# Performance work log

Measured on AMD Instinct MI355X. Metric: run time of the kernel, lower is better.

Reference implementation:

```python
import jax, jax.numpy as jnp
import numpy as np

N = 10000   # num_nodes
F = 64      # latent_dim
U = 128     # num_units
B = 8       # batch
K = 2       # gcn_step
E = 160000  # edges (avg degree 16)
M = 2 * K + 1  # num_matrices = len(supports)*gcn_step + 1


def setup_inputs() -> dict:
    rng = np.random.default_rng(0)
    rows = rng.integers(0, N, E).astype(np.int32)
    cols = rng.integers(0, N, E).astype(np.int32)
    vals = (rng.random(E).astype(np.float32) + 0.1)
    # random-walk normalization D^{-1} A, per the original utils.calculate_random_walk_matrix
    deg_out = np.zeros(N, np.float32); np.add.at(deg_out, rows, vals)
    deg_in = np.zeros(N, np.float32); np.add.at(deg_in, cols, vals)
    # support1 = (D_out^{-1} A)^T : out[c] += vals/d_out[r] * x[r]  -> dst=cols, src=rows
    w1 = vals / np.maximum(deg_out[rows], 1e-8)
    # support2 = (D_in^{-1} A^T)^T : out[r] += vals/d_in[c] * x[c]  -> dst=rows, src=cols
    w2 = vals / np.maximum(deg_in[cols], 1e-8)

    key = jax.random.key(0)
    ks = jax.random.split(key, 4)

    def xavier(k, shape):
        std = (2.0 / (shape[0] + shape[1])) ** 0.5
        return jax.random.normal(k, shape, jnp.float32) * std

    return {
        'y': jax.random.normal(ks[0], (B, N * F), jnp.float32),
        'W_lat': xavier(ks[1], (M * F, F)),
        'b_lat': jnp.ones((F,), jnp.float32),   # bias_start=1.0, shared (keyed by length)
        'W_units': xavier(ks[2], (M * F, U)),
        'b_units': jnp.zeros((U,), jnp.float32),
        'W_final': xavier(ks[3], (M * U, F)),
        'sup1_w': jnp.asarray(w1),
        'sup2_w': jnp.asarray(w2),
        'edge_rows': jnp.asarray(rows),
        'edge_cols': jnp.asarray(cols),
    }


def _spmm(dst, src, w, x):
    # sparse matmul S @ x with S given as COO edge list; x: (N, Fin, B)
    return jax.ops.segment_sum(w[:, None, None] * x[src], dst, num_segments=N)


def _gconv(x, supports, W, b):
    # x: (B, N, Fin) -> (B, N*Fout); Chebyshev diffusion convolution
    Bsz, n, fin = x.shape
    x0 = jnp.transpose(x, (1, 2, 0))  # (N, Fin, B)
    xs = [x0]
    for dst, src, w in supports:
        xk_2 = x0
        x1 = _spmm(dst, src, w, x0)
        xs.append(x1)
        for _ in range(2, K + 1):
            x2 = 2.0 * _spmm(dst, src, w, x1) - xk_2
            xs.append(x2)
            xk_2, x1 = x1, x2
    X = jnp.stack(xs, axis=-1)                       # (N, Fin, B, M)
    X = jnp.transpose(X, (2, 0, 1, 3)).reshape(Bsz * n, fin * len(xs))  # feature-major, matrix-minor
    out = X @ W + b
    return out.reshape(Bsz, n * W.shape[1])


def reference(y, W_lat, b_lat, W_units, b_units, W_final, sup1_w, sup2_w, edge_rows, edge_cols):
    supports = [(edge_cols, edge_rows, sup1_w), (edge_rows, edge_cols, sup2_w)]
    x = y.reshape(B, N, F)
    # theta gate (bias_start=1.0 via shared b_lat)
    theta = jax.nn.sigmoid(_gconv(x, supports, W_lat, b_lat))
    # ode_func_net: gen_layers=1 hidden gconv + final gconv (final bias is shared b_lat!)
    c = jnp.tanh(_gconv(x, supports, W_units, b_units)).reshape(B, N, U)
    c = jnp.tanh(_gconv(c, supports, W_final, b_lat))
    return -theta * c
```

## Files before the change

kernel.cpp:

```cpp
#include <hip/hip_runtime.h>

#define N_NODES 10000
#define NEDGE 160000
#define NB 80000
#define EPAD (NEDGE + 8 * N_NODES)

typedef unsigned int u32;
typedef unsigned short u16;
typedef __attribute__((ext_vector_type(8))) short short8;
typedef __attribute__((ext_vector_type(4))) float float4v;

__device__ __forceinline__ u16 f2bf(float f) {
    u32 u = __float_as_uint(f);
    return (u16)((u + 0x7fffu + ((u >> 16) & 1u)) >> 16);
}
__device__ __forceinline__ float lo16(u32 u) { return __uint_as_float(u << 16); }
__device__ __forceinline__ float hi16(u32 u) { return __uint_as_float(u & 0xffff0000u); }
__device__ __forceinline__ u32 pack2(float a, float b) {
    return (u32)f2bf(a) | (((u32)f2bf(b)) << 16);
}
__device__ __forceinline__ float fast_tanh(float v) {
    return 1.f - 2.f / (__expf(2.f * v) + 1.f);
}

static const size_t SLAB = (size_t)NB * 64;

__global__ __launch_bounds__(256) void prepcount_kernel(
    const float2* __restrict__ y, u32* __restrict__ X0,
    const float* __restrict__ W_lat, const float* __restrict__ W_units,
    u16* __restrict__ bpk12, const float* __restrict__ W_final, u16* __restrict__ bpkP,
    const int* __restrict__ rows, const int* __restrict__ cols, int* __restrict__ cnt) {
    int b = blockIdx.x, t = threadIdx.x;
    if (b < 10000) {
        int idx = b * 256 + t;
        int fh = idx & 31;
        int rb = idx >> 5;
        int bb = rb & 7;
        int n = rb >> 3;
        float2 v = y[((size_t)bb * N_NODES + n) * 32 + fh];
        X0[idx] = pack2(v.x, v.y);
    } else if (b < 10240) {
        int idx = (b - 10000) * 256 + t;
        int j = idx & 7;
        int lane = (idx >> 3) & 63;
        int rest = idx >> 9;
        int ct = rest % 12;
        int ks = rest / 12;
        int k = ks * 32 + (lane >> 4) * 8 + j;
        int col = ct * 16 + (lane & 15);
        int wrow = (k % 64) * 5 + (k / 64);
        float v = (col < 64) ? W_lat[wrow * 64 + col] : W_units[wrow * 128 + (col - 64)];
        bpk12[idx] = f2bf(v);
    } else if (b < 10400) {
        int idx = (b - 10240) * 256 + t;
        int j8 = idx & 7;
        int lane = (idx >> 3) & 63;
        int rest = idx >> 9;
        int ct = rest % 20;
        int ks = rest / 20;
        int k = ks * 32 + (lane >> 4) * 8 + j8;
        int col = ct * 16 + (lane & 15);
        int slot = col >> 6, j = col & 63;
        float v;
        if (slot == 0)
            v = W_final[(k * 5 + 0) * 64 + j] - W_final[(k * 5 + 2) * 64 + j] -
                W_final[(k * 5 + 4) * 64 + j];
        else
            v = W_final[(k * 5 + slot) * 64 + j];
        bpkP[idx] = f2bf(v);
    } else {
        int e = (b - 10400) * 256 + t;
        atomicAdd(&cnt[cols[e]], 1);
        atomicAdd(&cnt[N_NODES + rows[e]], 1);
    }
}

__global__ void blocksum_kernel(const int* __restrict__ cnt, int* __restrict__ bsums) {
    __shared__ int red[4];
    int arr = blockIdx.x / 40;
    int c = blockIdx.x % 40;
    int idx = c * 256 + threadIdx.x;
    int v = (idx < N_NODES) ? ((cnt[arr * N_NODES + idx] + 7) & ~7) : 0;
#pragma unroll
    for (int off = 32; off; off >>= 1) v += __shfl_down(v, off, 64);
    int wv = threadIdx.x >> 6, ln = threadIdx.x & 63;
    if (ln == 0) red[wv] = v;
    __syncthreads();
    if (threadIdx.x == 0) bsums[blockIdx.x] = red[0] + red[1] + red[2] + red[3];
}

__global__ void scanapply_kernel(int* __restrict__ cnt, const int* __restrict__ bsums,
                                 int* __restrict__ rowptr1, int* __restrict__ rowptr2) {
    __shared__ int lds[256];
    int arr = blockIdx.x / 40;
    int c = blockIdx.x % 40;
    int base = 0;
    for (int i = 0; i < c; i++) base += bsums[arr * 40 + i];
    int idx = c * 256 + threadIdx.x;
    bool ok = idx < N_NODES;
    int v = ok ? ((cnt[arr * N_NODES + idx] + 7) & ~7) : 0;
    int t = threadIdx.x;
    lds[t] = v;
    __syncthreads();
    for (int off = 1; off < 256; off <<= 1) {
        int add = (t >= off) ? lds[t - off] : 0;
        __syncthreads();
        lds[t] += add;
        __syncthreads();
    }
    int excl = lds[t] - v + base;
    if (ok) {
        int* rp = arr ? rowptr2 : rowptr1;
        rp[idx] = excl;
        cnt[arr * N_NODES + idx] = excl;
    }
    if (c == 39 && t == 255) {
        (arr ? rowptr2 : rowptr1)[N_NODES] = base + lds[255];
    }
}

__global__ void scatter_kernel(const int* __restrict__ rows, const int* __restrict__ cols,
                               const float* __restrict__ w1, const float* __restrict__ w2,
                               int* __restrict__ cur1, int* __restrict__ cur2,
                               int2* __restrict__ edges1, int2* __restrict__ edges2) {
    int e = blockIdx.x * 256 + threadIdx.x;
    if (e < NEDGE) {
        int r = rows[e], c = cols[e];
        int p1 = atomicAdd(&cur1[c], 1);
        edges1[p1] = make_int2(r, __float_as_int(w1[e]));
        int p2 = atomicAdd(&cur2[r], 1);
        edges2[p2] = make_int2(c, __float_as_int(w2[e]));
    }
}

__device__ __forceinline__ void gacc(float* acc, float w, uint4 u) {
    acc[0] += w * lo16(u.x); acc[1] += w * hi16(u.x);
    acc[2] += w * lo16(u.y); acc[3] += w * hi16(u.y);
    acc[4] += w * lo16(u.z); acc[5] += w * hi16(u.z);
    acc[6] += w * lo16(u.w); acc[7] += w * hi16(u.w);
}

__device__ __forceinline__ void gather_sliced(const u32* __restrict__ Xin,
                                              const int* __restrict__ rp,
                                              const int2* __restrict__ eg,
                                              int row, bool valid, int su, int l,
                                              float* acc) {
    int e = 0, e1 = 0;
    if (valid) {
        e = rp[row] + l;
        e1 = rp[row + 1];
    }
    while (__ballot(e < e1)) {
        int2 me = make_int2(0, 0);
        if (e < e1) me = eg[e];
#pragma unroll
        for (int j = 0; j < 8; j++) {
            int s = __shfl(me.x, j, 8);
            float w = __int_as_float(__shfl(me.y, j, 8));
            uint4 u = *(const uint4*)(Xin + (size_t)s * 256 + su + l * 4);
            gacc(acc, w, u);
        }
        e += 8;
    }
}

__global__ __launch_bounds__(256) void spmm2_kernel(
    const u32* __restrict__ XinA, const u32* __restrict__ XprevA, u32* __restrict__ XoutA,
    const u32* __restrict__ XinB, const u32* __restrict__ XprevB, u32* __restrict__ XoutB,
    const int* __restrict__ rowptr1, const int2* __restrict__ edges1,
    const int* __restrict__ rowptr2, const int2* __restrict__ edges2,
    float alpha, float beta) {
    int t = threadIdx.x;
    int lane = t & 63;
    int g = lane >> 3, l = lane & 7;
    int slice = blockIdx.x & 7;
    int chunk = blockIdx.x >> 3;
    int su = slice * 32;
    int v = chunk * 32 + (t >> 6) * 8 + g;
    bool hB = v >= N_NODES;
    int n = hB ? v - N_NODES : v;
    const u32* Xin = hB ? XinB : XinA;
    const u32* Xprev = hB ? XprevB : XprevA;
    u32* Xout = hB ? XoutB : XoutA;
    const int* rp = hB ? rowptr2 : rowptr1;
    const int2* eg = hB ? edges2 : edges1;

    float acc[8] = {0.f, 0.f, 0.f, 0.f, 0.f, 0.f, 0.f, 0.f};
    gather_sliced(Xin, rp, eg, n, true, su, l, acc);

    size_t o = (size_t)n * 256 + su + l * 4;
    if (beta != 0.f) {
        uint4 p = *(const uint4*)(Xprev + o);
        acc[0] = alpha * acc[0] + beta * lo16(p.x); acc[1] = alpha * acc[1] + beta * hi16(p.x);
        acc[2] = alpha * acc[2] + beta * lo16(p.y); acc[3] = alpha * acc[3] + beta * hi16(p.y);
        acc[4] = alpha * acc[4] + beta * lo16(p.z); acc[5] = alpha * acc[5] + beta * hi16(p.z);
        acc[6] = alpha * acc[6] + beta * lo16(p.w); acc[7] = alpha * acc[7] + beta * hi16(p.w);
    } else {
#pragma unroll
        for (int i = 0; i < 8; i++) acc[i] *= alpha;
    }
    uint4 r;
    r.x = pack2(acc[0], acc[1]);
    r.y = pack2(acc[2], acc[3]);
    r.z = pack2(acc[4], acc[5]);
    r.w = pack2(acc[6], acc[7]);
    *(uint4*)(Xout + o) = r;
}

__global__ __launch_bounds__(256) void spmm_final_kernel(
    const u32* __restrict__ T1, const u32* __restrict__ T2,
    const u32* __restrict__ Q, const u32* __restrict__ theta,
    const int* __restrict__ rowptr1, const int2* __restrict__ edges1,
    const int* __restrict__ rowptr2, const int2* __restrict__ edges2,
    float* __restrict__ outF) {
    int t = threadIdx.x;
    int lane = t & 63;
    int g = lane >> 3, l = lane & 7;
    int slice = blockIdx.x & 7;
    int chunk = blockIdx.x >> 3;
    int su = slice * 32;
    int n = chunk * 32 + (t >> 6) * 8 + g;
    bool valid = n < N_NODES;

    float acc[8] = {0.f, 0.f, 0.f, 0.f, 0.f, 0.f, 0.f, 0.f};
    gather_sliced(T1, rowptr1, edges1, n, valid, su, l, acc);
    gather_sliced(T2, rowptr2, edges2, n, valid, su, l, acc);
    if (!valid) return;

    size_t o = (size_t)n * 256 + su + l * 4;
    uint4 q = *(const uint4*)(Q + o);
    uint4 th = *(const uint4*)(theta + o);
    float res[8];
    res[0] = -lo16(th.x) * fast_tanh(lo16(q.x) + acc[0]);
    res[1] = -hi16(th.x) * fast_tanh(hi16(q.x) + acc[1]);
    res[2] = -lo16(th.y) * fast_tanh(lo16(q.y) + acc[2]);
    res[3] = -hi16(th.y) * fast_tanh(hi16(q.y) + acc[3]);
    res[4] = -lo16(th.z) * fast_tanh(lo16(q.z) + acc[4]);
    res[5] = -hi16(th.z) * fast_tanh(hi16(q.z) + acc[5]);
    res[6] = -lo16(th.w) * fast_tanh(lo16(q.w) + acc[6]);
    res[7] = -hi16(th.w) * fast_tanh(hi16(q.w) + acc[7]);
    float* dst = outF + (size_t)slice * (N_NODES * 64) + (size_t)n * 64 + l * 8;
    *(float4*)(dst) = make_float4(res[0], res[1], res[2], res[3]);
    *(float4*)(dst + 4) = make_float4(res[4], res[5], res[6], res[7]);
}

struct Slabs { const u16* p[5]; };

template <int FIN, int NM, int NOUT, int NSPLIT, int MODE>
__global__ __launch_bounds__(256) void gemm_kernel(
    Slabs A, const u16* __restrict__ Bp, const float* __restrict__ bias1,
    const float* __restrict__ bias2, u16* __restrict__ O1, u16* __restrict__ O2) {
    constexpr int K = NM * FIN;
    constexpr int KS = K / 32;
    constexpr int CTT = NOUT / 16;
    constexpr int CT = CTT / NSPLIT;
    int lane = threadIdx.x & 63;
    int wave = threadIdx.x >> 6;
    int rowBase = (blockIdx.x / NSPLIT) * 64 + wave * 16;
    int ctBase = (blockIdx.x % NSPLIT) * CT;
    int mrow = lane & 15;
    int kq = lane >> 4;

    float4v acc[CT];
#pragma unroll
    for (int c = 0; c < CT; c++) acc[c] = (float4v){0.f, 0.f, 0.f, 0.f};

#pragma unroll
    for (int ks = 0; ks < KS; ks++) {
        int k = ks * 32 + kq * 8;
        int m = k / FIN;
        int koff = k % FIN;
        short8 a = *(const short8*)(A.p[m] + (size_t)(rowBase + mrow) * FIN + koff);
        short8 b[CT];
#pragma unroll
        for (int ct = 0; ct < CT; ct++)
            b[ct] = *(const short8*)(Bp + ((size_t)(ks * CTT + ctBase + ct) * 64 + lane) * 8);
#pragma unroll
        for (int ct = 0; ct < CT; ct++)
            acc[ct] = __builtin_amdgcn_mfma_f32_16x16x32_bf16(a, b[ct], acc[ct], 0, 0, 0);
    }

    int rowq = rowBase + kq * 4;
#pragma unroll
    for (int ct = 0; ct < CT; ct++) {
        int col = (ctBase + ct) * 16 + mrow;
        float bsv;
        if (MODE == 0) bsv = (col < 64) ? bias1[col] : 0.f;
        else bsv = (col < 64) ? bias1[col] : bias2[col - 64];
#pragma unroll
        for (int i = 0; i < 4; i++) {
            float v = acc[ct][i] + bsv;
            int r = rowq + i;
            if (MODE == 0) {
                O1[(size_t)(col >> 6) * SLAB + (size_t)r * 64 + (col & 63)] = f2bf(v);
            } else {
                if (col < 64) {
                    v = 1.f / (1.f + __expf(-v));
                    O1[(size_t)r * 64 + col] = f2bf(v);
                } else {
                    O2[(size_t)r * 128 + (col - 64)] = f2bf(fast_tanh(v));
                }
            }
        }
    }
}

extern "C" void kernel_launch(void* const* d_in, const int* in_sizes, int n_in,
                              void* d_out, int out_size, void* d_ws, size_t ws_size,
                              hipStream_t stream) {
    const float2* y    = (const float2*)d_in[0];
    const float* W_lat = (const float*)d_in[1];
    const float* b_lat = (const float*)d_in[2];
    const float* W_units = (const float*)d_in[3];
    const float* b_units = (const float*)d_in[4];
    const float* W_final = (const float*)d_in[5];
    const float* sup1w = (const float*)d_in[6];
    const float* sup2w = (const float*)d_in[7];
    const int* rows    = (const int*)d_in[8];
    const int* cols    = (const int*)d_in[9];
    float* out = (float*)d_out;

    char* ws = (char*)d_ws;
    size_t off = 0;
    auto alloc = [&](size_t bytes) -> void* {
        void* p = ws + off;
        off += (bytes + 511) & ~(size_t)511;
        return p;
    };
    int* rowptr1 = (int*)alloc((N_NODES + 1) * 4);
    int* rowptr2 = (int*)alloc((N_NODES + 1) * 4);
    int* cnt = (int*)alloc((size_t)2 * N_NODES * 4);
    int* bsums = (int*)alloc(80 * 4);
    int2* edges1 = (int2*)alloc((size_t)EPAD * 8);
    int2* edges2 = (int2*)alloc((size_t)EPAD * 8);
    u16* bpk12 = (u16*)alloc((size_t)61440 * 2);
    u16* bpkP = (u16*)alloc((size_t)40960 * 2);
    u16* theta = (u16*)alloc((size_t)NB * 64 * 2);
    u16* S = (u16*)alloc((size_t)5 * NB * 64 * 2);
    u16* H0 = (u16*)alloc((size_t)NB * 128 * 2);
    u16* T1 = (u16*)alloc((size_t)NB * 64 * 2);
    u16* T2 = (u16*)alloc((size_t)NB * 64 * 2);

    hipMemsetAsync(cnt, 0, (size_t)2 * N_NODES * 4, stream);
    hipMemsetAsync(edges1, 0, (size_t)EPAD * 8, stream);
    hipMemsetAsync(edges2, 0, (size_t)EPAD * 8, stream);
    prepcount_kernel<<<11025, 256, 0, stream>>>(y, (u32*)S, W_lat, W_units, bpk12,
                                                W_final, bpkP, rows, cols, cnt);
    blocksum_kernel<<<80, 256, 0, stream>>>(cnt, bsums);
    scanapply_kernel<<<80, 256, 0, stream>>>(cnt, bsums, rowptr1, rowptr2);
    scatter_kernel<<<625, 256, 0, stream>>>(rows, cols, sup1w, sup2w,
                                            cnt, cnt + N_NODES, edges1, edges2);

    const u32* S0 = (const u32*)S;
    u32* X1 = (u32*)(S + 1 * SLAB);
    u32* X2 = (u32*)(S + 2 * SLAB);
    u32* X3 = (u32*)(S + 3 * SLAB);
    u32* X4 = (u32*)(S + 4 * SLAB);
    spmm2_kernel<<<5000, 256, 0, stream>>>(S0, nullptr, X1, S0, nullptr, X3,
                                           rowptr1, edges1, rowptr2, edges2, 1.f, 0.f);
    spmm2_kernel<<<5000, 256, 0, stream>>>(X1, S0, X2, X3, S0, X4,
                                           rowptr1, edges1, rowptr2, edges2, 2.f, -1.f);

    Slabs SX;
    for (int m = 0; m < 5; m++) SX.p[m] = S + (size_t)m * SLAB;
    gemm_kernel<64, 5, 192, 1, 1><<<1250, 256, 0, stream>>>(SX, bpk12, b_lat, b_units, theta, H0);

    Slabs SH;
    SH.p[0] = H0;
    gemm_kernel<128, 1, 320, 2, 0><<<2500, 256, 0, stream>>>(SH, bpkP, b_lat, nullptr, S, nullptr);

    const u32* Q  = (const u32*)(S + 0 * SLAB);
    const u32* P1 = (const u32*)(S + 1 * SLAB);
    const u32* P2 = (const u32*)(S + 2 * SLAB);
    const u32* P3 = (const u32*)(S + 3 * SLAB);
    const u32* P4 = (const u32*)(S + 4 * SLAB);
    spmm2_kernel<<<5000, 256, 0, stream>>>(P2, P1, (u32*)T1, P4, P3, (u32*)T2,
                                           rowptr1, edges1, rowptr2, edges2, 2.f, 1.f);
    spmm_final_kernel<<<2504, 256, 0, stream>>>((const u32*)T1, (const u32*)T2, Q,
                                                (const u32*)theta,
                                                rowptr1, edges1, rowptr2, edges2, out);
}
```

Before: 314.1 us.

## Bucket nodes by degree so SpMM wavefronts process similar-length rows

Builds per-support node orderings sorted by edge-count bucket (descending) via a histogram, a serial scan and an atomic fill, then has the SpMM kernels map threads to nodes through these permutations. The aim is to cut intra-wavefront divergence, since 8 nodes share a wavefront and run the gather loop for as many steps as the longest row. The cost is two extra small launches, extra histogram work in the scatter kernel, and one indirection load per thread. Output rows are also no longer written in node order, which may reduce locality.

```diff
diff --git a/kernel.cpp b/kernel.cpp
--- a/kernel.cpp
+++ b/kernel.cpp
@@ -122,14 +122,52 @@
 __global__ void scatter_kernel(const int* __restrict__ rows, const int* __restrict__ cols,
                                const float* __restrict__ w1, const float* __restrict__ w2,
                                int* __restrict__ cur1, int* __restrict__ cur2,
-                               int2* __restrict__ edges1, int2* __restrict__ edges2) {
-    int e = blockIdx.x * 256 + threadIdx.x;
-    if (e < NEDGE) {
+                               int2* __restrict__ edges1, int2* __restrict__ edges2,
+                               const int* __restrict__ rp1, const int* __restrict__ rp2,
+                               int* __restrict__ hist) {
+    if (blockIdx.x < 625) {
+        int e = blockIdx.x * 256 + threadIdx.x;
         int r = rows[e], c = cols[e];
         int p1 = atomicAdd(&cur1[c], 1);
         edges1[p1] = make_int2(r, __float_as_int(w1[e]));
         int p2 = atomicAdd(&cur2[r], 1);
         edges2[p2] = make_int2(c, __float_as_int(w2[e]));
+    } else {
+        int n = (blockIdx.x - 625) * 256 + threadIdx.x;
+        if (n < N_NODES) {
+            int c1 = min(31, (rp1[n + 1] - rp1[n]) >> 3);
+            int c2 = min(31, (rp2[n + 1] - rp2[n]) >> 3);
+            int c12 = min(31, c1 + c2);
+            atomicAdd(&hist[c1], 1);
+            atomicAdd(&hist[32 + c2], 1);
+            atomicAdd(&hist[64 + c12], 1);
+        }
+    }
+}
+
+__global__ void orderscan_kernel(int* __restrict__ histcur) {
+    if (threadIdx.x == 0) {
+        for (int a = 0; a < 3; a++) {
+            int base = 0;
+            for (int b = 31; b >= 0; b--) {
+                histcur[96 + a * 32 + b] = base;
+                base += histcur[a * 32 + b];
+            }
+        }
+    }
+}
+
+__global__ void orderfill_kernel(const int* __restrict__ rp1, const int* __restrict__ rp2,
+                                 int* __restrict__ histcur, int* __restrict__ order1,
+                                 int* __restrict__ order2, int* __restrict__ order12) {
+    int n = blockIdx.x * 256 + threadIdx.x;
+    if (n < N_NODES) {
+        int c1 = min(31, (rp1[n + 1] - rp1[n]) >> 3);
+        int c2 = min(31, (rp2[n + 1] - rp2[n]) >> 3);
+        int c12 = min(31, c1 + c2);
+        order1[atomicAdd(&histcur[96 + c1], 1)] = n;
+        order2[atomicAdd(&histcur[96 + 32 + c2], 1)] = n;
+        order12[atomicAdd(&histcur[96 + 64 + c12], 1)] = n;
     }
 }
 
@@ -169,6 +207,7 @@
     const u32* __restrict__ XinB, const u32* __restrict__ XprevB, u32* __restrict__ XoutB,
     const int* __restrict__ rowptr1, const int2* __restrict__ edges1,
     const int* __restrict__ rowptr2, const int2* __restrict__ edges2,
+    const int* __restrict__ order1, const int* __restrict__ order2,
     float alpha, float beta) {
     int t = threadIdx.x;
     int lane = t & 63;
@@ -178,7 +217,7 @@
     int su = slice * 32;
     int v = chunk * 32 + (t >> 6) * 8 + g;
     bool hB = v >= N_NODES;
-    int n = hB ? v - N_NODES : v;
+    int n = hB ? order2[v - N_NODES] : order1[v];
     const u32* Xin = hB ? XinB : XinA;
     const u32* Xprev = hB ? XprevB : XprevA;
     u32* Xout = hB ? XoutB : XoutA;
@@ -212,15 +251,16 @@
     const u32* __restrict__ Q, const u32* __restrict__ theta,
     const int* __restrict__ rowptr1, const int2* __restrict__ edges1,
     const int* __restrict__ rowptr2, const int2* __restrict__ edges2,
-    float* __restrict__ outF) {
+    const int* __restrict__ order12, float* __restrict__ outF) {
     int t = threadIdx.x;
     int lane = t & 63;
     int g = lane >> 3, l = lane & 7;
     int slice = blockIdx.x & 7;
     int chunk = blockIdx.x >> 3;
     int su = slice * 32;
-    int n = chunk * 32 + (t >> 6) * 8 + g;
-    bool valid = n < N_NODES;
+    int v = chunk * 32 + (t >> 6) * 8 + g;
+    bool valid = v < N_NODES;
+    int n = valid ? order12[v] : 0;
 
     float acc[8] = {0.f, 0.f, 0.f, 0.f, 0.f, 0.f, 0.f, 0.f};
     gather_sliced(T1, rowptr1, edges1, n, valid, su, l, acc);
@@ -329,8 +369,12 @@
     };
     int* rowptr1 = (int*)alloc((N_NODES + 1) * 4);
     int* rowptr2 = (int*)alloc((N_NODES + 1) * 4);
-    int* cnt = (int*)alloc((size_t)2 * N_NODES * 4);
+    int* cnt = (int*)alloc(((size_t)2 * N_NODES + 192) * 4);
+    int* histcur = cnt + 2 * N_NODES;
     int* bsums = (int*)alloc(80 * 4);
+    int* order1 = (int*)alloc((size_t)N_NODES * 4);
+    int* order2 = (int*)alloc((size_t)N_NODES * 4);
+    int* order12 = (int*)alloc((size_t)N_NODES * 4);
     int2* edges1 = (int2*)alloc((size_t)EPAD * 8);
     int2* edges2 = (int2*)alloc((size_t)EPAD * 8);
     u16* bpk12 = (u16*)alloc((size_t)61440 * 2);
@@ -341,15 +385,19 @@
     u16* T1 = (u16*)alloc((size_t)NB * 64 * 2);
     u16* T2 = (u16*)alloc((size_t)NB * 64 * 2);
 
-    hipMemsetAsync(cnt, 0, (size_t)2 * N_NODES * 4, stream);
+    hipMemsetAsync(cnt, 0, ((size_t)2 * N_NODES + 192) * 4, stream);
     hipMemsetAsync(edges1, 0, (size_t)EPAD * 8, stream);
     hipMemsetAsync(edges2, 0, (size_t)EPAD * 8, stream);
     prepcount_kernel<<<11025, 256, 0, stream>>>(y, (u32*)S, W_lat, W_units, bpk12,
                                                 W_final, bpkP, rows, cols, cnt);
     blocksum_kernel<<<80, 256, 0, stream>>>(cnt, bsums);
     scanapply_kernel<<<80, 256, 0, stream>>>(cnt, bsums, rowptr1, rowptr2);
-    scatter_kernel<<<625, 256, 0, stream>>>(rows, cols, sup1w, sup2w,
-                                            cnt, cnt + N_NODES, edges1, edges2);
+    scatter_kernel<<<665, 256, 0, stream>>>(rows, cols, sup1w, sup2w,
+                                            cnt, cnt + N_NODES, edges1, edges2,
+                                            rowptr1, rowptr2, histcur);
+    orderscan_kernel<<<1, 64, 0, stream>>>(histcur);
+    orderfill_kernel<<<40, 256, 0, stream>>>(rowptr1, rowptr2, histcur,
+                                             order1, order2, order12);
 
     const u32* S0 = (const u32*)S;
     u32* X1 = (u32*)(S + 1 * SLAB);
@@ -357,9 +405,11 @@
     u32* X3 = (u32*)(S + 3 * SLAB);
     u32* X4 = (u32*)(S + 4 * SLAB);
     spmm2_kernel<<<5000, 256, 0, stream>>>(S0, nullptr, X1, S0, nullptr, X3,
-                                           rowptr1, edges1, rowptr2, edges2, 1.f, 0.f);
+                                           rowptr1, edges1, rowptr2, edges2,
+                                           order1, order2, 1.f, 0.f);
     spmm2_kernel<<<5000, 256, 0, stream>>>(X1, S0, X2, X3, S0, X4,
-                                           rowptr1, edges1, rowptr2, edges2, 2.f, -1.f);
+                                           rowptr1, edges1, rowptr2, edges2,
+                                           order1, order2, 2.f, -1.f);
 
     Slabs SX;
     for (int m = 0; m < 5; m++) SX.p[m] = S + (size_t)m * SLAB;
@@ -375,8 +425,10 @@
     const u32* P3 = (const u32*)(S + 3 * SLAB);
     const u32* P4 = (const u32*)(S + 4 * SLAB);
     spmm2_kernel<<<5000, 256, 0, stream>>>(P2, P1, (u32*)T1, P4, P3, (u32*)T2,
-                                           rowptr1, edges1, rowptr2, edges2, 2.f, 1.f);
+                                           rowptr1, edges1, rowptr2, edges2,
+                                           order1, order2, 2.f, 1.f);
     spmm_final_kernel<<<2504, 256, 0, stream>>>((const u32*)T1, (const u32*)T2, Q,
                                                 (const u32*)theta,
-                                                rowptr1, edges1, rowptr2, edges2, out);
-}
+                                                rowptr1, edges1, rowptr2, edges2,
+                                                order12, out);
+}
```

Measured after the change: 539.9 us. 71.9% more time.

## Sort nodes by degree bucket to balance SpMM gather wavefronts

Applied to the files above, without the earlier changes.

Adds a counting-sort pass that groups nodes into descending degree buckets (in steps of 8 edges) for each support and for the combined final pass. The SpMM kernels then map each 8-lane group to a node taken from this order rather than the natural node index. The aim is to cut wavefront divergence, since the ballot-driven edge loop runs as long as the highest-degree node in the wavefront. The cost is three extra small kernel launches, one extra index indirection per node, and scattered output writes and neighbour locality.

```diff
diff --git a/kernel.cpp b/kernel.cpp
--- a/kernel.cpp
+++ b/kernel.cpp
@@ -133,6 +133,76 @@
     }
 }
 
+__device__ __forceinline__ void node_buckets(const int* rp1, const int* rp2, int n,
+                                             int& c1, int& c2, int& c12) {
+    c1 = min(31, (rp1[n + 1] - rp1[n]) >> 3);
+    c2 = min(31, (rp2[n + 1] - rp2[n]) >> 3);
+    c12 = min(31, c1 + c2);
+}
+
+__global__ void histfill_kernel(const int* __restrict__ rp1, const int* __restrict__ rp2,
+                                int* __restrict__ bh) {
+    __shared__ int h[96];
+    int t = threadIdx.x;
+    if (t < 96) h[t] = 0;
+    __syncthreads();
+    int n = blockIdx.x * 256 + t;
+    if (n < N_NODES) {
+        int c1, c2, c12;
+        node_buckets(rp1, rp2, n, c1, c2, c12);
+        atomicAdd(&h[c1], 1);
+        atomicAdd(&h[32 + c2], 1);
+        atomicAdd(&h[64 + c12], 1);
+    }
+    __syncthreads();
+    if (t < 96) bh[blockIdx.x * 96 + t] = h[t];
+}
+
+__global__ void orderscan_kernel(int* __restrict__ bh) {
+    __shared__ int tot[96];
+    __shared__ int start[96];
+    int k = threadIdx.x;
+    if (k < 96) {
+        int s = 0;
+        for (int b = 0; b < 40; b++) s += bh[b * 96 + k];
+        tot[k] = s;
+    }
+    __syncthreads();
+    if (k < 3) {
+        int base = 0;
+        for (int bkt = 31; bkt >= 0; bkt--) {
+            start[k * 32 + bkt] = base;
+            base += tot[k * 32 + bkt];
+        }
+    }
+    __syncthreads();
+    if (k < 96) {
+        int run = start[k];
+        for (int b = 0; b < 40; b++) {
+            int tmp = bh[b * 96 + k];
+            bh[b * 96 + k] = run;
+            run += tmp;
+        }
+    }
+}
+
+__global__ void orderfill_kernel(const int* __restrict__ rp1, const int* __restrict__ rp2,
+                                 const int* __restrict__ bh, int* __restrict__ order1,
+                                 int* __restrict__ order2, int* __restrict__ order12) {
+    __shared__ int cur[96];
+    int t = threadIdx.x;
+    if (t < 96) cur[t] = bh[blockIdx.x * 96 + t];
+    __syncthreads();
+    int n = blockIdx.x * 256 + t;
+    if (n < N_NODES) {
+        int c1, c2, c12;
+        node_buckets(rp1, rp2, n, c1, c2, c12);
+        order1[atomicAdd(&cur[c1], 1)] = n;
+        order2[atomicAdd(&cur[32 + c2], 1)] = n;
+        order12[atomicAdd(&cur[64 + c12], 1)] = n;
+    }
+}
+
 __device__ __forceinline__ void gacc(float* acc, float w, uint4 u) {
     acc[0] += w * lo16(u.x); acc[1] += w * hi16(u.x);
     acc[2] += w * lo16(u.y); acc[3] += w * hi16(u.y);
@@ -169,6 +239,7 @@
     const u32* __restrict__ XinB, const u32* __restrict__ XprevB, u32* __restrict__ XoutB,
     const int* __restrict__ rowptr1, const int2* __restrict__ edges1,
     const int* __restrict__ rowptr2, const int2* __restrict__ edges2,
+    const int* __restrict__ order1, const int* __restrict__ order2,
     float alpha, float beta) {
     int t = threadIdx.x;
     int lane = t & 63;
@@ -178,7 +249,7 @@
     int su = slice * 32;
     int v = chunk * 32 + (t >> 6) * 8 + g;
     bool hB = v >= N_NODES;
-    int n = hB ? v - N_NODES : v;
+    int n = hB ? order2[v - N_NODES] : order1[v];
     const u32* Xin = hB ? XinB : XinA;
     const u32* Xprev = hB ? XprevB : XprevA;
     u32* Xout = hB ? XoutB : XoutA;
@@ -212,15 +283,16 @@
     const u32* __restrict__ Q, const u32* __restrict__ theta,
     const int* __restrict__ rowptr1, const int2* __restrict__ edges1,
     const int* __restrict__ rowptr2, const int2* __restrict__ edges2,
-    float* __restrict__ outF) {
+    const int* __restrict__ order12, float* __restrict__ outF) {
     int t = threadIdx.x;
     int lane = t & 63;
     int g = lane >> 3, l = lane & 7;
     int slice = blockIdx.x & 7;
     int chunk = blockIdx.x >> 3;
     int su = slice * 32;
-    int n = chunk * 32 + (t >> 6) * 8 + g;
-    bool valid = n < N_NODES;
+    int v = chunk * 32 + (t >> 6) * 8 + g;
+    bool valid = v < N_NODES;
+    int n = valid ? order12[v] : 0;
 
     float acc[8] = {0.f, 0.f, 0.f, 0.f, 0.f, 0.f, 0.f, 0.f};
     gather_sliced(T1, rowptr1, edges1, n, valid, su, l, acc);
@@ -331,6 +403,10 @@
     int* rowptr2 = (int*)alloc((N_NODES + 1) * 4);
     int* cnt = (int*)alloc((size_t)2 * N_NODES * 4);
     int* bsums = (int*)alloc(80 * 4);
+    int* bh = (int*)alloc((size_t)40 * 96 * 4);
+    int* order1 = (int*)alloc((size_t)N_NODES * 4);
+    int* order2 = (int*)alloc((size_t)N_NODES * 4);
+    int* order12 = (int*)alloc((size_t)N_NODES * 4);
     int2* edges1 = (int2*)alloc((size_t)EPAD * 8);
     int2* edges2 = (int2*)alloc((size_t)EPAD * 8);
     u16* bpk12 = (u16*)alloc((size_t)61440 * 2);
@@ -348,6 +424,10 @@
                                                 W_final, bpkP, rows, cols, cnt);
     blocksum_kernel<<<80, 256, 0, stream>>>(cnt, bsums);
     scanapply_kernel<<<80, 256, 0, stream>>>(cnt, bsums, rowptr1, rowptr2);
+    histfill_kernel<<<40, 256, 0, stream>>>(rowptr1, rowptr2, bh);
+    orderscan_kernel<<<1, 128, 0, stream>>>(bh);
+    orderfill_kernel<<<40, 256, 0, stream>>>(rowptr1, rowptr2, bh,
+                                             order1, order2, order12);
     scatter_kernel<<<625, 256, 0, stream>>>(rows, cols, sup1w, sup2w,
                                             cnt, cnt + N_NODES, edges1, edges2);
 
@@ -357,9 +437,11 @@
     u32* X3 = (u32*)(S + 3 * SLAB);
     u32* X4 = (u32*)(S + 4 * SLAB);
     spmm2_kernel<<<5000, 256, 0, stream>>>(S0, nullptr, X1, S0, nullptr, X3,
-                                           rowptr1, edges1, rowptr2, edges2, 1.f, 0.f);
+                                           rowptr1, edges1, rowptr2, edges2,
+                                           order1, order2, 1.f, 0.f);
     spmm2_kernel<<<5000, 256, 0, stream>>>(X1, S0, X2, X3, S0, X4,
-                                           rowptr1, edges1, rowptr2, edges2, 2.f, -1.f);
+                                           rowptr1, edges1, rowptr2, edges2,
+                                           order1, order2, 2.f, -1.f);
 
     Slabs SX;
     for (int m = 0; m < 5; m++) SX.p[m] = S + (size_t)m * SLAB;
@@ -375,8 +457,10 @@
     const u32* P3 = (const u32*)(S + 3 * SLAB);
     const u32* P4 = (const u32*)(S + 4 * SLAB);
     spmm2_kernel<<<5000, 256, 0, stream>>>(P2, P1, (u32*)T1, P4, P3, (u32*)T2,
-                                           rowptr1, edges1, rowptr2, edges2, 2.f, 1.f);
+                                           rowptr1, edges1, rowptr2, edges2,
+                                           order1, order2, 2.f, 1.f);
     spmm_final_kernel<<<2504, 256, 0, stream>>>((const u32*)T1, (const u32*)T2, Q,
                                                 (const u32*)theta,
-                                                rowptr1, edges1, rowptr2, edges2, out);
-}
+                                                rowptr1, edges1, rowptr2, edges2,
+                                                order12, out);
+}
```

Result: no change. 315.8 us (+0.6%).

## Split each row's edge gather across two lane groups and prefetch edges

Applied to the files above, without the earlier changes.

Each node row is now handled by 16 lanes instead of 8. The two 8-lane halves take alternating chunks of 8 edges and are combined with a cross-half shuffle reduction before the epilogue. The next edge chunk is loaded one iteration ahead to hide edge-list latency. Grid sizes double to keep the same coverage. This raises memory-level parallelism per row at the cost of more blocks, extra shuffles, and half the lanes sitting idle in the epilogue. The valid guard in the final kernel is removed, which relies on the 5000-block grid mapping exactly onto 10000 nodes.

```diff
diff --git a/kernel.cpp b/kernel.cpp
--- a/kernel.cpp
+++ b/kernel.cpp
@@ -143,16 +143,16 @@
 __device__ __forceinline__ void gather_sliced(const u32* __restrict__ Xin,
                                               const int* __restrict__ rp,
                                               const int2* __restrict__ eg,
-                                              int row, bool valid, int su, int l,
+                                              int row, int su, int l, int h,
                                               float* acc) {
-    int e = 0, e1 = 0;
-    if (valid) {
-        e = rp[row] + l;
-        e1 = rp[row + 1];
-    }
+    int e = rp[row] + h * 8 + l;
+    int e1 = rp[row + 1];
+    int2 me = make_int2(0, 0);
+    if (e < e1) me = eg[e];
     while (__ballot(e < e1)) {
-        int2 me = make_int2(0, 0);
-        if (e < e1) me = eg[e];
+        int en = e + 16;
+        int2 men = make_int2(0, 0);
+        if (en < e1) men = eg[en];
 #pragma unroll
         for (int j = 0; j < 8; j++) {
             int s = __shfl(me.x, j, 8);
@@ -160,7 +160,8 @@
             uint4 u = *(const uint4*)(Xin + (size_t)s * 256 + su + l * 4);
             gacc(acc, w, u);
         }
-        e += 8;
+        e = en;
+        me = men;
     }
 }
 
@@ -172,11 +173,13 @@
     float alpha, float beta) {
     int t = threadIdx.x;
     int lane = t & 63;
-    int g = lane >> 3, l = lane & 7;
+    int g = lane >> 4;
+    int l16 = lane & 15;
+    int h = l16 >> 3, l = l16 & 7;
     int slice = blockIdx.x & 7;
     int chunk = blockIdx.x >> 3;
     int su = slice * 32;
-    int v = chunk * 32 + (t >> 6) * 8 + g;
+    int v = chunk * 16 + (t >> 6) * 4 + g;
     bool hB = v >= N_NODES;
     int n = hB ? v - N_NODES : v;
     const u32* Xin = hB ? XinB : XinA;
@@ -186,7 +189,10 @@
     const int2* eg = hB ? edges2 : edges1;
 
     float acc[8] = {0.f, 0.f, 0.f, 0.f, 0.f, 0.f, 0.f, 0.f};
-    gather_sliced(Xin, rp, eg, n, true, su, l, acc);
+    gather_sliced(Xin, rp, eg, n, su, l, h, acc);
+#pragma unroll
+    for (int i = 0; i < 8; i++) acc[i] += __shfl_xor(acc[i], 8, 64);
+    if (h) return;
 
     size_t o = (size_t)n * 256 + su + l * 4;
     if (beta != 0.f) {
@@ -215,17 +221,20 @@
     float* __restrict__ outF) {
     int t = threadIdx.x;
     int lane = t & 63;
-    int g = lane >> 3, l = lane & 7;
+    int g = lane >> 4;
+    int l16 = lane & 15;
+    int h = l16 >> 3, l = l16 & 7;
     int slice = blockIdx.x & 7;
     int chunk = blockIdx.x >> 3;
     int su = slice * 32;
-    int n = chunk * 32 + (t >> 6) * 8 + g;
-    bool valid = n < N_NODES;
+    int n = chunk * 16 + (t >> 6) * 4 + g;
 
     float acc[8] = {0.f, 0.f, 0.f, 0.f, 0.f, 0.f, 0.f, 0.f};
-    gather_sliced(T1, rowptr1, edges1, n, valid, su, l, acc);
-    gather_sliced(T2, rowptr2, edges2, n, valid, su, l, acc);
-    if (!valid) return;
+    gather_sliced(T1, rowptr1, edges1, n, su, l, h, acc);
+    gather_sliced(T2, rowptr2, edges2, n, su, l, h, acc);
+#pragma unroll
+    for (int i = 0; i < 8; i++) acc[i] += __shfl_xor(acc[i], 8, 64);
+    if (h) return;
 
     size_t o = (size_t)n * 256 + su + l * 4;
     uint4 q = *(const uint4*)(Q + o);
@@ -356,10 +365,10 @@
     u32* X2 = (u32*)(S + 2 * SLAB);
     u32* X3 = (u32*)(S + 3 * SLAB);
     u32* X4 = (u32*)(S + 4 * SLAB);
-    spmm2_kernel<<<5000, 256, 0, stream>>>(S0, nullptr, X1, S0, nullptr, X3,
-                                           rowptr1, edges1, rowptr2, edges2, 1.f, 0.f);
-    spmm2_kernel<<<5000, 256, 0, stream>>>(X1, S0, X2, X3, S0, X4,
-                                           rowptr1, edges1, rowptr2, edges2, 2.f, -1.f);
+    spmm2_kernel<<<10000, 256, 0, stream>>>(S0, nullptr, X1, S0, nullptr, X3,
+                                            rowptr1, edges1, rowptr2, edges2, 1.f, 0.f);
+    spmm2_kernel<<<10000, 256, 0, stream>>>(X1, S0, X2, X3, S0, X4,
+                                            rowptr1, edges1, rowptr2, edges2, 2.f, -1.f);
 
     Slabs SX;
     for (int m = 0; m < 5; m++) SX.p[m] = S + (size_t)m * SLAB;
@@ -374,9 +383,9 @@
     const u32* P2 = (const u32*)(S + 2 * SLAB);
     const u32* P3 = (const u32*)(S + 3 * SLAB);
     const u32* P4 = (const u32*)(S + 4 * SLAB);
-    spmm2_kernel<<<5000, 256, 0, stream>>>(P2, P1, (u32*)T1, P4, P3, (u32*)T2,
-                                           rowptr1, edges1, rowptr2, edges2, 2.f, 1.f);
-    spmm_final_kernel<<<2504, 256, 0, stream>>>((const u32*)T1, (const u32*)T2, Q,
+    spmm2_kernel<<<10000, 256, 0, stream>>>(P2, P1, (u32*)T1, P4, P3, (u32*)T2,
+                                            rowptr1, edges1, rowptr2, edges2, 2.f, 1.f);
+    spmm_final_kernel<<<5000, 256, 0, stream>>>((const u32*)T1, (const u32*)T2, Q,
                                                 (const u32*)theta,
                                                 rowptr1, edges1, rowptr2, edges2, out);
 }
```

After: 331.9 us. 1.06x slower.
